# Kernel tuning notes

Hardware: AMD Instinct MI355X
Metric: run time of the kernel (lower is better)

Reference implementation:

```python
import jax, jax.numpy as jnp
import numpy as np

E, N, D, H = 500000, 100000, 8, 256
BN_EPS = 1e-5


def _batchnorm(x, gamma, beta):
    # BatchNorm1d in training mode: biased batch statistics over dim 0
    mu = jnp.mean(x, axis=0)
    var = jnp.var(x, axis=0)
    return (x - mu) * jax.lax.rsqrt(var + BN_EPS) * gamma + beta


def _encoder(x, W1, b1, gamma, beta, W2, b2):
    h = jax.nn.relu(x @ W1 + b1)
    h = _batchnorm(h, gamma, beta)
    return h @ W2 + b2


def setup_inputs() -> dict:
    key = jax.random.key(0)
    ks = jax.random.split(key, 24)
    s = 0.05  # weight init scale
    inp = {
        "edge_attr": jax.random.normal(ks[0], (E, D), dtype=jnp.float32),
        "node_features": jax.random.normal(ks[1], (N, D), dtype=jnp.float32),
        "edge_index": jax.random.randint(ks[2], (2, E), 0, N, dtype=jnp.int32),
        "e_W1": jax.random.normal(ks[3], (D, H)) * s,
        "e_b1": jax.random.normal(ks[4], (H,)) * s,
        "e_gamma": jnp.ones((H,), jnp.float32),
        "e_beta": jnp.zeros((H,), jnp.float32),
        "e_W2": jax.random.normal(ks[5], (H, H)) * s,
        "e_b2": jax.random.normal(ks[6], (H,)) * s,
        "n_W1": jax.random.normal(ks[7], (D, H)) * s,
        "n_b1": jax.random.normal(ks[8], (H,)) * s,
        "n_gamma": jnp.ones((H,), jnp.float32),
        "n_beta": jnp.zeros((H,), jnp.float32),
        "n_W2": jax.random.normal(ks[9], (H, H)) * s,
        "n_b2": jax.random.normal(ks[10], (H,)) * s,
        "Wv": jax.random.normal(ks[11], (H, H)) * s,
        "bv": jax.random.normal(ks[12], (H,)) * s,
        "Wo": jax.random.normal(ks[13], (H, H)) * s,
        "bo": jax.random.normal(ks[14], (H,)) * s,
        "Wp": jax.random.normal(ks[15], (H, D)) * s,
        "bp": jax.random.normal(ks[16], (D,)) * s,
    }
    return inp


def reference(edge_attr, node_features, edge_index,
              e_W1, e_b1, e_gamma, e_beta, e_W2, e_b2,
              n_W1, n_b1, n_gamma, n_beta, n_W2, n_b2,
              Wv, bv, Wo, bo, Wp, bp):
    # edge encoder: Linear -> ReLU -> BatchNorm1d -> Linear
    edge_encoded = _encoder(edge_attr, e_W1, e_b1, e_gamma, e_beta, e_W2, e_b2)

    # gather endpoint features and average (node dim == edge dim, slice is no-op)
    src = node_features[edge_index[0]]  # [E, D]
    tgt = node_features[edge_index[1]]  # [E, D]
    node_context = (src + tgt) * 0.5
    node_encoded = _encoder(node_context, n_W1, n_b1, n_gamma, n_beta, n_W2, n_b2)

    # MultiheadAttention with seq_len=1: softmax over one key is exactly 1,
    # so output = out_proj(v_proj(node_encoded)); q/k projections cancel.
    attn_out = (node_encoded @ Wv + bv) @ Wo + bo  # [E, H]

    edge_attr_enhanced = attn_out @ Wp + bp  # [E, D]
    return edge_attr + 0.5 * edge_attr_enhanced
```

## Files before the change

### kernel.cpp

```cpp
#include <hip/hip_runtime.h>
#include <hip/hip_bf16.h>
#include <string.h>

#define E_CNT 500000
#define N_CNT 100000
#define HID   256
#define NTILE 31250

typedef short short8 __attribute__((ext_vector_type(8)));
typedef float f32x4 __attribute__((ext_vector_type(4)));

__device__ __forceinline__ unsigned short f2bf(float f){
  union { float f; unsigned int i; } v; v.f = f;
  unsigned int u = v.i;
  u = u + 0x7FFFu + ((u >> 16) & 1u);
  return (unsigned short)(u >> 16);
}

__device__ __forceinline__ unsigned int pk_bf16(float a, float b){
  __hip_bfloat162 p = __float22bfloat162_rn(make_float2(a, b));
  unsigned int u; memcpy(&u, &p, 4); return u;
}

__device__ __forceinline__ void init_w1_lds(unsigned short* w1l,
                                            const float* W1, const float* b1,
                                            int tid){
  int ch = tid;
  #pragma unroll
  for (int j = 0; j < 8; ++j){
    unsigned short w = f2bf(W1[j * HID + ch]);
    w1l[ch * 24 + j]     = w;
    w1l[ch * 24 + 8 + j] = w;
  }
  w1l[ch * 24 + 16] = f2bf(2.0f * b1[ch]);
  #pragma unroll
  for (int j = 17; j < 24; ++j) w1l[ch * 24 + j] = 0;
  if (tid < 32) w1l[256 * 24 + tid] = 0;
}

__global__ __launch_bounds__(256, 3) void k1_stats(
    const int* __restrict__ eidx, const float* __restrict__ nf,
    const float* __restrict__ W1, const float* __restrict__ b1,
    float* __restrict__ part, float* __restrict__ bd2)
{
  __shared__ unsigned short w1l[256 * 24 + 32];
  __shared__ unsigned short ctx[4][16 * 40];
  __shared__ float sred[2][4][128];

  const int tid = threadIdx.x, lane = tid & 63, wid = tid >> 6;
  const int cg = wid & 1;
  const int pair = (blockIdx.x * 4 + wid) >> 1;
  const int npair = gridDim.x * 2;
  const int m = lane & 15, q = lane >> 4;
  const int r = lane >> 2, side = (lane >> 1) & 1, half = lane & 1;

  if (blockIdx.x == 0 && tid < 16) bd2[tid] = 0.f;

  init_w1_lds(w1l, W1, b1, tid);

  unsigned short* myctx = ctx[wid];
  for (int i = lane; i < 16 * 40; i += 64) myctx[i] = 0;
  if (lane < 16) myctx[lane * 40 + 16] = 0x3F80;
  __syncthreads();

  short8 w1fr[8];
  #pragma unroll
  for (int nt = 0; nt < 8; ++nt)
    w1fr[nt] = *(const short8*)&w1l[((cg * 8 + nt) * 16 + m) * 24 + q * 8];

  const f32x4 z4 = {0.f, 0.f, 0.f, 0.f};
  f32x4 sacc[8], qacc[8];
  #pragma unroll
  for (int nt = 0; nt < 8; ++nt){ sacc[nt] = z4; qacc[nt] = z4; }

  int t = pair;
  float4 nfc = make_float4(0.f,0.f,0.f,0.f); int i1 = 0;
  if (t < NTILE){
    int id0 = eidx[side * E_CNT + t * 16 + r];
    nfc = ((const float4*)nf)[id0 * 2 + half];
  }
  { int tn = t + npair;
    if (tn < NTILE) i1 = eidx[side * E_CNT + tn * 16 + r]; }

  for (; t < NTILE; t += npair){
    *(uint2*)&myctx[r * 40 + side * 8 + half * 4] =
        make_uint2(pk_bf16(nfc.x, nfc.y), pk_bf16(nfc.z, nfc.w));

    int tn1 = t + npair, tn2 = t + 2 * npair;
    float4 nfn = make_float4(0.f,0.f,0.f,0.f); int i2 = 0;
    if (tn1 < NTILE) nfn = ((const float4*)nf)[i1 * 2 + half];
    if (tn2 < NTILE) i2 = eidx[side * E_CNT + tn2 * 16 + r];

    asm volatile("s_waitcnt lgkmcnt(0)" ::: "memory");
    short8 bfr = *(const short8*)&myctx[m * 40 + q * 8];
    #pragma unroll
    for (int nt = 0; nt < 8; ++nt){
      f32x4 c = __builtin_amdgcn_mfma_f32_16x16x32_bf16(w1fr[nt], bfr, z4, 0, 0, 0);
      f32x4 hv = __builtin_elementwise_max(c, z4);
      sacc[nt] += hv;
      qacc[nt] += hv * hv;
    }
    nfc = nfn; i1 = i2;
  }

  #pragma unroll
  for (int nt = 0; nt < 8; ++nt){
    #pragma unroll
    for (int i = 0; i < 4; ++i){
      float v = sacc[nt][i], w = qacc[nt][i];
      v += __shfl_xor(v, 1); w += __shfl_xor(w, 1);
      v += __shfl_xor(v, 2); w += __shfl_xor(w, 2);
      v += __shfl_xor(v, 4); w += __shfl_xor(w, 4);
      v += __shfl_xor(v, 8); w += __shfl_xor(w, 8);
      if (m == 0){
        int loc = nt * 16 + q * 4 + i;
        sred[0][wid][loc] = v;
        sred[1][wid][loc] = w;
      }
    }
  }
  __syncthreads();
  {
    int j = tid, hf = j >> 7, loc = j & 127;
    float s0 = sred[0][hf][loc] + sred[0][hf + 2][loc];
    float s1 = sred[1][hf][loc] + sred[1][hf + 2][loc];
    part[blockIdx.x * 512 + j]       = s0;
    part[blockIdx.x * 512 + 256 + j] = s1;
  }
}

__global__ __launch_bounds__(64) void kRow(const float* __restrict__ W,
                                           const float* __restrict__ X,
                                           float* __restrict__ Y)
{
  const int r = blockIdx.x, t = threadIdx.x;
  float4 w4 = ((const float4*)(W + r * HID))[t];
  float wv[4] = {w4.x, w4.y, w4.z, w4.w};
  float acc[8];
  #pragma unroll
  for (int d = 0; d < 8; ++d) acc[d] = 0.f;
  #pragma unroll
  for (int dj = 0; dj < 4; ++dj){
    int j = 4 * t + dj;
    float4 x0 = ((const float4*)(X + j * 8))[0];
    float4 x1 = ((const float4*)(X + j * 8))[1];
    acc[0] = fmaf(wv[dj], x0.x, acc[0]); acc[1] = fmaf(wv[dj], x0.y, acc[1]);
    acc[2] = fmaf(wv[dj], x0.z, acc[2]); acc[3] = fmaf(wv[dj], x0.w, acc[3]);
    acc[4] = fmaf(wv[dj], x1.x, acc[4]); acc[5] = fmaf(wv[dj], x1.y, acc[5]);
    acc[6] = fmaf(wv[dj], x1.z, acc[6]); acc[7] = fmaf(wv[dj], x1.w, acc[7]);
  }
  #pragma unroll
  for (int d = 0; d < 8; ++d){
    acc[d] += __shfl_xor(acc[d], 1);
    acc[d] += __shfl_xor(acc[d], 2);
    acc[d] += __shfl_xor(acc[d], 4);
    acc[d] += __shfl_xor(acc[d], 8);
    acc[d] += __shfl_xor(acc[d], 16);
    acc[d] += __shfl_xor(acc[d], 32);
  }
  if (t < 8) Y[r * 8 + t] = acc[t];
}

__global__ __launch_bounds__(256) void kC(
    const float* __restrict__ part, int nb,
    const float* __restrict__ gamma, const float* __restrict__ beta,
    const float* __restrict__ nW2,
    const float* __restrict__ T1s, const float* __restrict__ T2s,
    const float* __restrict__ Wp,
    const float* __restrict__ bv, const float* __restrict__ bo,
    const float* __restrict__ bp, const float* __restrict__ nb2,
    unsigned short* __restrict__ wd2t, float* __restrict__ bd2)
{
  __shared__ float T2L[2048];
  __shared__ float scr[2048];
  __shared__ float stL[8];
  const int t = threadIdx.x, b = blockIdx.x;

  for (int i = t; i < 2048; i += 256) T2L[i] = T2s[i];

  {
    int cl = t >> 6, i = t & 63;
    int c = b * 4 + cl;
    float s0 = 0.f, s1 = 0.f;
    for (int b2 = i; b2 < nb; b2 += 64){
      s0 += part[b2 * 512 + c];
      s1 += part[b2 * 512 + 256 + c];
    }
    scr[cl * 128 + i]      = s0;
    scr[cl * 128 + 64 + i] = s1;
  }
  __syncthreads();
  if (t < 4){
    float s0 = 0.f, s1 = 0.f;
    for (int i = 0; i < 64; ++i){
      s0 += scr[t * 128 + i];
      s1 += scr[t * 128 + 64 + i];
    }
    const float invE = 1.0f / (float)E_CNT;
    float mu  = s0 * invE;
    float var = fmaxf(s1 * invE - mu * mu, 0.f);
    float s   = gamma[b * 4 + t] * rsqrtf(var + 4.0f * 1e-5f);
    stL[t]     = s;
    stL[4 + t] = beta[b * 4 + t] - mu * s;
  }
  __syncthreads();

  {
    int cl = t >> 6, d = (t >> 3) & 7, p8 = t & 7;
    int c = b * 4 + cl;
    const float* row = nW2 + c * HID;
    float a = 0.f;
    for (int j = p8 * 32; j < p8 * 32 + 32; ++j)
      a = fmaf(row[j], T2L[j * 8 + d], a);
    scr[t] = a;
  }
  __syncthreads();
  {
    int cl = t >> 6, d = (t >> 3) & 7, p8 = t & 7;
    if (p8 == 0){
      float w = 0.f;
      #pragma unroll
      for (int i = 0; i < 8; ++i) w += scr[t + i];
      int c = b * 4 + cl;
      wd2t[d * HID + c]       = f2bf(0.5f * stL[cl] * w);
      wd2t[(8 + d) * HID + c] = 0;
      scr[1024 + cl * 8 + d]  = stL[4 + cl] * w;
    }
  }
  __syncthreads();
  if (t < 8){
    float a = scr[1024 + t] + scr[1024 + 8 + t] +
              scr[1024 + 16 + t] + scr[1024 + 24 + t];
    #pragma unroll
    for (int jj = 0; jj < 4; ++jj){
      int j = 4 * b + jj;
      a = fmaf(nb2[j], T2L[j * 8 + t], a);
      a = fmaf(bv[j],  T1s[j * 8 + t], a);
      a = fmaf(bo[j],  Wp[j * 8 + t], a);
    }
    if (b == 0) a += bp[t];
    atomicAdd(&bd2[t], a);
  }
}

__global__ __launch_bounds__(256, 3) void k3_main(
    const int* __restrict__ eidx, const float* __restrict__ nf,
    const float* __restrict__ ea,
    const float* __restrict__ W1, const float* __restrict__ b1,
    const unsigned short* __restrict__ wd2t, const float* __restrict__ bd2,
    float* __restrict__ out)
{
  __shared__ unsigned short w1l[256 * 24 + 32];
  __shared__ unsigned short ctx[4][16 * 40];
  __shared__ unsigned short hbuf[4][16 * 264];

  const int tid = threadIdx.x, lane = tid & 63, wid = tid >> 6;
  const int gw = blockIdx.x * 4 + wid, ngw = gridDim.x * 4;
  const int m = lane & 15, q = lane >> 4;
  const int r = lane >> 2, side = (lane >> 1) & 1, half = lane & 1;

  init_w1_lds(w1l, W1, b1, tid);

  short8 w2fr[8];
  #pragma unroll
  for (int kb = 0; kb < 8; ++kb)
    w2fr[kb] = *(const short8*)&wd2t[m * HID + kb * 32 + q * 8];
  const float bd2v = (m < 8) ? 0.5f * bd2[m] : 0.f;

  unsigned short* myctx = ctx[wid];
  unsigned short* myh   = hbuf[wid];
  for (int i = lane; i < 16 * 40; i += 64) myctx[i] = 0;
  if (lane < 16) myctx[lane * 40 + 16] = 0x3F80;
  __syncthreads();

  short8 w1fr[16];
  #pragma unroll
  for (int nt = 0; nt < 16; ++nt)
    w1fr[nt] = *(const short8*)&w1l[(nt * 16 + m) * 24 + q * 8];

  const f32x4 z4 = {0.f, 0.f, 0.f, 0.f};

  int t = gw;
  float4 nfc = make_float4(0.f,0.f,0.f,0.f); int i1 = 0;
  if (t < NTILE){
    int id0 = eidx[side * E_CNT + t * 16 + r];
    nfc = ((const float4*)nf)[id0 * 2 + half];
  }
  { int tn = t + ngw;
    if (tn < NTILE) i1 = eidx[side * E_CNT + tn * 16 + r]; }

  const bool dok = (m < 8);
  for (; t < NTILE; t += ngw){
    *(uint2*)&myctx[r * 40 + side * 8 + half * 4] =
        make_uint2(pk_bf16(nfc.x, nfc.y), pk_bf16(nfc.z, nfc.w));

    float eav[4];
    #pragma unroll
    for (int i = 0; i < 4; ++i)
      eav[i] = dok ? ea[(t * 16 + q * 4 + i) * 8 + m] : 0.f;

    int tn1 = t + ngw, tn2 = t + 2 * ngw;
    float4 nfn = make_float4(0.f,0.f,0.f,0.f); int i2 = 0;
    if (tn1 < NTILE) nfn = ((const float4*)nf)[i1 * 2 + half];
    if (tn2 < NTILE) i2 = eidx[side * E_CNT + tn2 * 16 + r];

    asm volatile("s_waitcnt lgkmcnt(0)" ::: "memory");
    short8 bfr = *(const short8*)&myctx[m * 40 + q * 8];
    #pragma unroll
    for (int nt = 0; nt < 16; ++nt){
      f32x4 c = __builtin_amdgcn_mfma_f32_16x16x32_bf16(w1fr[nt], bfr, z4, 0, 0, 0);
      f32x4 hv = __builtin_elementwise_max(c, z4);
      *(uint2*)&myh[m * 264 + nt * 16 + q * 4] =
          make_uint2(pk_bf16(hv[0], hv[1]), pk_bf16(hv[2], hv[3]));
    }
    asm volatile("s_waitcnt lgkmcnt(0)" ::: "memory");
    f32x4 acc = z4;
    #pragma unroll
    for (int kb = 0; kb < 8; ++kb){
      short8 afr = *(const short8*)&myh[m * 264 + kb * 32 + q * 8];
      acc = __builtin_amdgcn_mfma_f32_16x16x32_bf16(afr, w2fr[kb], acc, 0, 0, 0);
    }
    if (dok){
      #pragma unroll
      for (int i = 0; i < 4; ++i){
        float o = eav[i] + acc[i] + bd2v;
        out[(t * 16 + q * 4 + i) * 8 + m] = o;
      }
    }
    nfc = nfn; i1 = i2;
  }
}

extern "C" void kernel_launch(void* const* d_in, const int* in_sizes, int n_in,
                              void* d_out, int out_size, void* d_ws, size_t ws_size,
                              hipStream_t stream)
{
  const float* ea   = (const float*)d_in[0];
  const float* nf   = (const float*)d_in[1];
  const int*   eidx = (const int*)d_in[2];
  const float* nW1    = (const float*)d_in[9];
  const float* nb1    = (const float*)d_in[10];
  const float* ngamma = (const float*)d_in[11];
  const float* nbeta  = (const float*)d_in[12];
  const float* nW2    = (const float*)d_in[13];
  const float* nb2    = (const float*)d_in[14];
  const float* Wv     = (const float*)d_in[15];
  const float* bv     = (const float*)d_in[16];
  const float* Wo     = (const float*)d_in[17];
  const float* bo     = (const float*)d_in[18];
  const float* Wp     = (const float*)d_in[19];
  const float* bp     = (const float*)d_in[20];

  long avail = (long)ws_size - 8192 - 64 - 16384;
  int nb = (int)(avail / 2048);
  if (nb > 768) nb = 768;
  if (nb < 1)   nb = 1;

  char* ws = (char*)d_ws;
  size_t off = (size_t)nb * 2048;
  float* ws_part          = (float*)(ws + 0);
  unsigned short* ws_wd2t = (unsigned short*)(ws + off);
  float* ws_bd2           = (float*)(ws + off + 8192);
  float* ws_t1            = (float*)(ws + off + 8192 + 64);
  float* ws_t2            = (float*)(ws + off + 8192 + 64 + 8192);

  k1_stats<<<dim3(nb), dim3(256), 0, stream>>>(eidx, nf, nW1, nb1,
                                               ws_part, ws_bd2);
  kRow<<<dim3(256), dim3(64), 0, stream>>>(Wo, Wp, ws_t1);
  kRow<<<dim3(256), dim3(64), 0, stream>>>(Wv, ws_t1, ws_t2);
  kC<<<dim3(64), dim3(256), 0, stream>>>(
      ws_part, nb, ngamma, nbeta, nW2, ws_t1, ws_t2, Wp, bv, bo, bp, nb2,
      ws_wd2t, ws_bd2);
  k3_main<<<dim3(768), dim3(256), 0, stream>>>(
      eidx, nf, ea, nW1, nb1, ws_wd2t, ws_bd2, (float*)d_out);
}
```

Measured before the change: 184.7 us.

## Chain MFMA outputs directly as next MFMA operands, dropping LDS hidden buffer

The hidden activations from the first GEMM are no longer written to and reread from LDS. The output fragments of two first-stage MFMAs are packed to bf16 and used directly as the B operand of the second-stage MFMA. For this to work the second GEMM is transposed and the weight fragment is permuted to match the MFMA output layout. The output and edge_attr accesses become float4 per lane. This removes LDS traffic and two waitcnt stalls and frees LDS for occupancy, in exchange for a more intricate register layout that must match exactly.

Result: no change. 185.4 us (+0.4%).

```diff
diff --git a/kernel.cpp b/kernel.cpp
--- a/kernel.cpp
+++ b/kernel.cpp
@@ -252,7 +252,6 @@
 {
   __shared__ unsigned short w1l[256 * 24 + 32];
   __shared__ unsigned short ctx[4][16 * 40];
-  __shared__ unsigned short hbuf[4][16 * 264];
 
   const int tid = threadIdx.x, lane = tid & 63, wid = tid >> 6;
   const int gw = blockIdx.x * 4 + wid, ngw = gridDim.x * 4;
@@ -261,14 +260,20 @@
 
   init_w1_lds(w1l, W1, b1, tid);
 
-  short8 w2fr[8];
-  #pragma unroll
-  for (int kb = 0; kb < 8; ++kb)
-    w2fr[kb] = *(const short8*)&wd2t[m * HID + kb * 32 + q * 8];
-  const float bd2v = (m < 8) ? 0.5f * bd2[m] : 0.f;
+  short8 wA[8];
+  #pragma unroll
+  for (int kb = 0; kb < 8; ++kb){
+    short8 a;
+    #pragma unroll
+    for (int j = 0; j < 8; ++j){
+      int c = (2 * kb + (j >> 2)) * 16 + q * 4 + (j & 3);
+      a[j] = (short)wd2t[m * HID + c];
+    }
+    wA[kb] = a;
+  }
+  f32x4 bd2v = 0.5f * ((const f32x4*)bd2)[q & 3];
 
   unsigned short* myctx = ctx[wid];
-  unsigned short* myh   = hbuf[wid];
   for (int i = lane; i < 16 * 40; i += 64) myctx[i] = 0;
   if (lane < 16) myctx[lane * 40 + 16] = 0x3F80;
   __syncthreads();
@@ -289,15 +294,13 @@
   { int tn = t + ngw;
     if (tn < NTILE) i1 = eidx[side * E_CNT + tn * 16 + r]; }
 
-  const bool dok = (m < 8);
+  const bool dok = (q < 2);
   for (; t < NTILE; t += ngw){
     *(uint2*)&myctx[r * 40 + side * 8 + half * 4] =
         make_uint2(pk_bf16(nfc.x, nfc.y), pk_bf16(nfc.z, nfc.w));
 
-    float eav[4];
-    #pragma unroll
-    for (int i = 0; i < 4; ++i)
-      eav[i] = dok ? ea[(t * 16 + q * 4 + i) * 8 + m] : 0.f;
+    float4 eav = make_float4(0.f,0.f,0.f,0.f);
+    if (dok) eav = *(const float4*)&ea[(t * 16 + m) * 8 + q * 4];
 
     int tn1 = t + ngw, tn2 = t + 2 * ngw;
     float4 nfn = make_float4(0.f,0.f,0.f,0.f); int i2 = 0;
@@ -306,26 +309,27 @@
 
     asm volatile("s_waitcnt lgkmcnt(0)" ::: "memory");
     short8 bfr = *(const short8*)&myctx[m * 40 + q * 8];
-    #pragma unroll
-    for (int nt = 0; nt < 16; ++nt){
-      f32x4 c = __builtin_amdgcn_mfma_f32_16x16x32_bf16(w1fr[nt], bfr, z4, 0, 0, 0);
-      f32x4 hv = __builtin_elementwise_max(c, z4);
-      *(uint2*)&myh[m * 264 + nt * 16 + q * 4] =
-          make_uint2(pk_bf16(hv[0], hv[1]), pk_bf16(hv[2], hv[3]));
-    }
-    asm volatile("s_waitcnt lgkmcnt(0)" ::: "memory");
+
     f32x4 acc = z4;
     #pragma unroll
     for (int kb = 0; kb < 8; ++kb){
-      short8 afr = *(const short8*)&myh[m * 264 + kb * 32 + q * 8];
-      acc = __builtin_amdgcn_mfma_f32_16x16x32_bf16(afr, w2fr[kb], acc, 0, 0, 0);
+      f32x4 c0 = __builtin_amdgcn_mfma_f32_16x16x32_bf16(w1fr[2*kb],   bfr, z4, 0, 0, 0);
+      f32x4 c1 = __builtin_amdgcn_mfma_f32_16x16x32_bf16(w1fr[2*kb+1], bfr, z4, 0, 0, 0);
+      f32x4 h0 = __builtin_elementwise_max(c0, z4);
+      f32x4 h1 = __builtin_elementwise_max(c1, z4);
+      union { short8 s; unsigned int u[4]; } bu;
+      bu.u[0] = pk_bf16(h0[0], h0[1]);
+      bu.u[1] = pk_bf16(h0[2], h0[3]);
+      bu.u[2] = pk_bf16(h1[0], h1[1]);
+      bu.u[3] = pk_bf16(h1[2], h1[3]);
+      acc = __builtin_amdgcn_mfma_f32_16x16x32_bf16(wA[kb], bu.s, acc, 0, 0, 0);
     }
     if (dok){
-      #pragma unroll
-      for (int i = 0; i < 4; ++i){
-        float o = eav[i] + acc[i] + bd2v;
-        out[(t * 16 + q * 4 + i) * 8 + m] = o;
-      }
+      float4 o = make_float4(eav.x + acc[0] + bd2v[0],
+                             eav.y + acc[1] + bd2v[1],
+                             eav.z + acc[2] + bd2v[2],
+                             eav.w + acc[3] + bd2v[3]);
+      *(float4*)&out[(t * 16 + m) * 8 + q * 4] = o;
     }
     nfc = nfn; i1 = i2;
   }
```
